# Optimization experiments

Measured on AMD Instinct MI355X. Metric: run time of the kernel, lower is better.

The kernel has to match this reference:

```python
import jax, jax.numpy as jnp
import numpy as np

ALPHAS = [2.0 ** k for k in range(-3, 2)]  # cfg.model.mmd.alphas = 2.0
EPS = 1e-12


def _center(x):
    return x - x.mean(axis=-1, keepdims=True)


def _l2norm(x):
    return x / jnp.sqrt(jnp.sum(x * x, axis=-1, keepdims=True) + EPS)


def _multi_gauss(d2):
    # sum_a exp(-a * d2), fused over the alpha list
    out = jnp.exp(-ALPHAS[0] * d2)
    for a in ALPHAS[1:]:
        out = out + jnp.exp(-a * d2)
    return out


def _sq_dists_self(x):
    # x: [..., n, c] -> squared euclidean pairwise [..., n, n]
    sq = jnp.sum(x * x, axis=-1)  # [..., n]
    gram = jnp.einsum('...ic,...jc->...ij', x, x)
    d2 = sq[..., :, None] + sq[..., None, :] - 2.0 * gram
    return jnp.maximum(d2, 0.0)


def setup_inputs() -> dict:
    key = jax.random.key(0)
    k1, k2 = jax.random.split(key)
    support_xf = jax.random.normal(k1, (16, 5, 130, 640), dtype=jnp.float32)
    query_xf = jax.random.normal(k2, (16, 75, 25, 640), dtype=jnp.float32)
    return {"support_xf": support_xf, "query_xf": query_xf}


def reference(support_xf, query_xf):
    # support_xf: [b, n_way, ns, c], query_xf: [b, q, nq, c]
    b, n_way, ns, c = support_xf.shape
    _, q, nq, _ = query_xf.shape

    # centering over feature dim, then l2 norm (cfg.model.mmd.l2norm = True)
    s = _l2norm(_center(support_xf))
    t = _l2norm(_center(query_xf))

    # self Gram kernels
    k_ss = _multi_gauss(_sq_dists_self(s))  # [b, n_way, ns, ns]
    k_qq = _multi_gauss(_sq_dists_self(t))  # [b, q, nq, nq]

    # cross kernel: broadcast instead of materializing expanded 5D copies
    sn = jnp.sum(s * s, axis=-1)  # [b, n_way, ns]
    tn = jnp.sum(t * t, axis=-1)  # [b, q, nq]
    gram_qs = jnp.einsum('bwsc,bqtc->bqwst', s, t)  # [b, q, n_way, ns, nq]
    d2_qs = jnp.maximum(
        sn[:, None, :, :, None] + tn[:, :, None, None, :] - 2.0 * gram_qs, 0.0)
    k_qs = _multi_gauss(d2_qs)

    # MMD terms: unbiased self terms drop the diagonal
    mmd_s = (jnp.sum(k_ss, axis=(-1, -2)) - jnp.trace(k_ss, axis1=-2, axis2=-1)) \
        / (ns * (ns - 1))  # [b, n_way]
    mmd_q = (jnp.sum(k_qq, axis=(-1, -2)) - jnp.trace(k_qq, axis1=-2, axis2=-1)) \
        / (nq * (nq - 1))  # [b, q]
    mmd_qs = jnp.sum(k_qs, axis=(-1, -2)) / (ns * nq)  # [b, q, n_way]

    mmd_dis = mmd_s[:, None, :] + mmd_q[:, :, None] - 2.0 * mmd_qs  # [b, q, n_way]
    return mmd_dis
```

## Files before the change

kernel.cpp:

```cpp
#include <hip/hip_runtime.h>
#include <math.h>


#define EXP_C (-0.25f * 1.44269504088896340736f)

typedef __attribute__((ext_vector_type(8))) short bf16x8_t;
typedef __attribute__((ext_vector_type(4))) float f32x4_t;
typedef unsigned short u16;

#define GLOAD_LDS16(g, l)                                 \
  __builtin_amdgcn_global_load_lds(                       \
      (const __attribute__((address_space(1))) void*)(g), \
      (__attribute__((address_space(3))) void*)(l), 16, 0, 0)

__device__ __forceinline__ u16 f2bf(float f) {
  unsigned int u = __float_as_uint(f);
  unsigned int r = (u + 0x7fffu + ((u >> 16) & 1u)) >> 16;
  return (u16)r;
}

__device__ __forceinline__ float mgauss(float g) {
  float h = fmaxf(1.f - g, 0.f);
  float e1 = exp2f(h * EXP_C);
  float e2 = e1 * e1, e4 = e2 * e2, e8 = e4 * e4, e16 = e8 * e8;
  return e1 + e2 + e4 + e8 + e16;
}

__device__ __forceinline__ float wred(float v) {
#pragma unroll
  for (int m = 1; m < 64; m <<= 1) v += __shfl_xor(v, m, 64);
  return v;
}

__global__ void prep_kernel(const float* __restrict__ S,
                            const float* __restrict__ Q,
                            u16* __restrict__ SHL, u16* __restrict__ QHL,
                            float* __restrict__ accz) {
  int bid = blockIdx.x, tid = threadIdx.x;
  if (bid < 29) {
    int z = bid * 256 + tid;
    if (z < 7280) accz[z] = 0.f;
  }
  int wid = (bid << 2) | (tid >> 6);
  int lane = tid & 63;
  const float* src;
  u16* dst;
  if (wid < 10400) {
    src = S + (size_t)wid * 640;
    dst = SHL + (size_t)wid * 640;
  } else {
    int w2 = wid - 10400;
    src = Q + (size_t)w2 * 640;
    dst = QHL + (size_t)w2 * 640;
  }
  const float4* s4 = (const float4*)src;
  float4 a = s4[lane];
  float4 b = s4[lane + 64];
  float4 c = make_float4(0.f, 0.f, 0.f, 0.f);
  if (lane < 32) c = s4[lane + 128];
  float s = a.x + a.y + a.z + a.w + b.x + b.y + b.z + b.w + c.x + c.y + c.z +
            c.w;
  float ss = a.x * a.x + a.y * a.y + a.z * a.z + a.w * a.w + b.x * b.x +
             b.y * b.y + b.z * b.z + b.w * b.w + c.x * c.x + c.y * c.y +
             c.z * c.z + c.w * c.w;
#pragma unroll
  for (int m = 1; m < 64; m <<= 1) {
    s += __shfl_xor(s, m, 64);
    ss += __shfl_xor(ss, m, 64);
  }
  float mean = s * (1.f / 640.f);
  float inv = 1.f / sqrtf(fmaxf(ss - s * s * (1.f / 640.f), 0.f) + 1e-12f);
  ushort4* d4 = (ushort4*)dst;
  d4[lane] = make_ushort4(f2bf((a.x - mean) * inv), f2bf((a.y - mean) * inv),
                          f2bf((a.z - mean) * inv), f2bf((a.w - mean) * inv));
  d4[lane + 64] =
      make_ushort4(f2bf((b.x - mean) * inv), f2bf((b.y - mean) * inv),
                   f2bf((b.z - mean) * inv), f2bf((b.w - mean) * inv));
  if (lane < 32)
    d4[lane + 128] =
        make_ushort4(f2bf((c.x - mean) * inv), f2bf((c.y - mean) * inv),
                     f2bf((c.z - mean) * inv), f2bf((c.w - mean) * inv));
}

__global__ __launch_bounds__(256, 2) void grams_kernel(
    const u16* __restrict__ SHL, const u16* __restrict__ QHL,
    float* __restrict__ accS, float* __restrict__ accQ,
    float* __restrict__ accQS) {
  __shared__ __align__(16) u16 sA[2][128 * 64];
  __shared__ __align__(16) u16 sB[2][128 * 64];
  const int bid = blockIdx.x;
  const int id = (bid & 7) * 242 + (bid >> 3);
  const int tid = threadIdx.x;
  const int w = tid >> 6, l = tid & 63;

  int mode, gb, i0, j0, nx, ny;
  const u16 *pX, *pY;
  if (id < 1440) {
    mode = 0;
    gb = id / 90;
    int r = id % 90;
    i0 = (r % 6) * 128;
    j0 = (r / 6) * 128;
    pX = SHL + (size_t)gb * 650 * 640;
    pY = QHL + (size_t)gb * 1875 * 640;
    nx = 650;
    ny = 1875;
  } else if (id < 1696) {
    mode = 1;
    int t = id - 1440;
    gb = t >> 4;
    int p = t & 15;
    int ti, tj;
    if (p < 4) {
      ti = p >> 1;
      tj = p & 1;
    } else {
      int q = (p - 4) / 3, r3 = (p - 4) % 3;
      ti = (r3 == 0) ? q + 1 : q + 2;
      tj = (r3 == 1) ? q + 1 : q + 2;
    }
    i0 = ti * 128;
    j0 = tj * 128;
    pX = pY = SHL + (size_t)gb * 650 * 640;
    nx = ny = 650;
  } else {
    mode = 2;
    gb = id - 1696;
    i0 = 0;
    j0 = 0;
    pX = pY = QHL + (size_t)gb * 125 * 640;
    nx = ny = 125;
  }

  const u16* gA[4];
  const u16* gB[4];
#pragma unroll
  for (int i = 0; i < 4; ++i) {
    int s = (w * 4 + i) * 64 + l;
    int r = s >> 3;
    int c16 = ((s & 7) ^ (r & 7)) * 8;
    int vi = i0 + r;
    vi = vi < nx ? vi : nx - 1;
    gA[i] = pX + (size_t)vi * 640 + c16;
    int vj = j0 + r;
    vj = vj < ny ? vj : ny - 1;
    gB[i] = pY + (size_t)vj * 640 + c16;
  }

  f32x4_t av[4][4];
#pragma unroll
  for (int i = 0; i < 4; ++i)
#pragma unroll
    for (int j = 0; j < 4; ++j)
#pragma unroll
      for (int r = 0; r < 4; ++r) av[i][j][r] = 0.f;

  const int wr = w >> 1, wc = w & 1;
  const int R0 = wr * 64, C0 = wc * 64;
  const int lr = l & 15, lk8 = (l >> 4) * 8;

#define STAGE(bb, c)                                          \
  {                                                           \
    int kb = (c) * 64;                                        \
    _Pragma("unroll") for (int i = 0; i < 4; ++i) {           \
      GLOAD_LDS16(gA[i] + kb, &sA[bb][(w * 4 + i) * 512]);    \
      GLOAD_LDS16(gB[i] + kb, &sB[bb][(w * 4 + i) * 512]);    \
    }                                                         \
  }

#define COMPUTE(bb)                                                           \
  {                                                                           \
    _Pragma("unroll") for (int ks = 0; ks < 2; ++ks) {                        \
      bf16x8_t af[4], bfv[4];                                                 \
      int kk = ks * 32 + lk8;                                                 \
      _Pragma("unroll") for (int t = 0; t < 4; ++t) {                         \
        int rr = R0 + t * 16 + lr;                                            \
        af[t] = *(const bf16x8_t*)&sA[bb][rr * 64 + (kk ^ ((rr & 7) << 3))];  \
        int cc = C0 + t * 16 + lr;                                            \
        bfv[t] = *(const bf16x8_t*)&sB[bb][cc * 64 + (kk ^ ((cc & 7) << 3))]; \
      }                                                                       \
      _Pragma("unroll") for (int i = 0; i < 4; ++i)                           \
          _Pragma("unroll") for (int j = 0; j < 4; ++j) av[i][j] =            \
          __builtin_amdgcn_mfma_f32_16x16x32_bf16(af[i], bfv[j], av[i][j], 0, \
                                                  0, 0);                      \
    }                                                                         \
  }

  STAGE(0, 0);
  __syncthreads();
  for (int c = 0; c < 10; ++c) {
    if (c < 9) STAGE((c + 1) & 1, c + 1);
    COMPUTE(c & 1);
    __syncthreads();
  }
#undef STAGE
#undef COMPUTE

  int gcv[4];
  bool cvv[4];
#pragma unroll
  for (int j = 0; j < 4; ++j) {
    gcv[j] = j0 + C0 + j * 16 + lr;
    cvv[j] = gcv[j] < ny;
  }

  if (mode == 0) {
    const int cbi = (i0 + R0) / 130;
    const int cbj = (j0 + C0) / 25;
    int cjr[4];
#pragma unroll
    for (int j = 0; j < 4; ++j) cjr[j] = gcv[j] / 25 - cbj;
    float ce[2][4] = {{0.f, 0.f, 0.f, 0.f}, {0.f, 0.f, 0.f, 0.f}};
#pragma unroll
    for (int i = 0; i < 4; ++i)
#pragma unroll
      for (int rr = 0; rr < 4; ++rr) {
        int gr = i0 + R0 + i * 16 + (l >> 4) * 4 + rr;
        bool rv = gr < 650;
        bool ra = (gr / 130) == cbi;
#pragma unroll
        for (int j = 0; j < 4; ++j) {
          float kv = mgauss(av[i][j][rr]);
          kv = (rv && cvv[j]) ? kv : 0.f;
          float k0 = ra ? kv : 0.f;
          ce[0][j] += k0;
          ce[1][j] += kv - k0;
        }
      }
#pragma unroll
    for (int a = 0; a < 2; ++a)
#pragma unroll
      for (int bq = 0; bq < 4; ++bq) {
        float t = 0.f;
#pragma unroll
        for (int j = 0; j < 4; ++j) t += (cjr[j] == bq) ? ce[a][j] : 0.f;
        t = wred(t);
        if (l == 0) {
          int ci = cbi + a, cj = cbj + bq;
          if (ci < 5 && cj < 75) atomicAdd(&accQS[gb * 375 + cj * 5 + ci], t);
        }
      }
  } else if (mode == 1) {
    const int cbi = (i0 + R0) / 130;
    int ccv[4];
#pragma unroll
    for (int j = 0; j < 4; ++j) ccv[j] = gcv[j] / 130;
    float ce[2][4] = {{0.f, 0.f, 0.f, 0.f}, {0.f, 0.f, 0.f, 0.f}};
#pragma unroll
    for (int i = 0; i < 4; ++i)
#pragma unroll
      for (int rr = 0; rr < 4; ++rr) {
        int gr = i0 + R0 + i * 16 + (l >> 4) * 4 + rr;
        bool rv = gr < 650;
        int rc = gr / 130;
        bool ra = rc == cbi;
#pragma unroll
        for (int j = 0; j < 4; ++j) {
          float kv = mgauss(av[i][j][rr]);
          bool val = rv && cvv[j] && (ccv[j] == rc) && (gr != gcv[j]);
          kv = val ? kv : 0.f;
          float k0 = ra ? kv : 0.f;
          ce[0][j] += k0;
          ce[1][j] += kv - k0;
        }
      }
#pragma unroll
    for (int a = 0; a < 2; ++a) {
      float t = wred(ce[a][0] + ce[a][1] + ce[a][2] + ce[a][3]);
      if (l == 0) {
        int ci = cbi + a;
        if (ci < 5) atomicAdd(&accS[gb * 5 + ci], t);
      }
    }
  } else {
    const int cbi = R0 / 25;
    int ccv[4];
#pragma unroll
    for (int j = 0; j < 4; ++j) ccv[j] = gcv[j] / 25;
    float ce[4][4] = {{0.f, 0.f, 0.f, 0.f},
                      {0.f, 0.f, 0.f, 0.f},
                      {0.f, 0.f, 0.f, 0.f},
                      {0.f, 0.f, 0.f, 0.f}};
#pragma unroll
    for (int i = 0; i < 4; ++i)
#pragma unroll
      for (int rr = 0; rr < 4; ++rr) {
        int gr = R0 + i * 16 + (l >> 4) * 4 + rr;
        bool rv = gr < 125;
        int rc = gr / 25;
        int ar = rc - cbi;
#pragma unroll
        for (int j = 0; j < 4; ++j) {
          float kv = mgauss(av[i][j][rr]);
          bool val = rv && cvv[j] && (ccv[j] == rc) && (gr != gcv[j]);
          kv = val ? kv : 0.f;
#pragma unroll
          for (int a = 0; a < 4; ++a) ce[a][j] += (ar == a) ? kv : 0.f;
        }
      }
#pragma unroll
    for (int a = 0; a < 4; ++a) {
      float t = wred(ce[a][0] + ce[a][1] + ce[a][2] + ce[a][3]);
      if (l == 0) {
        int ci = cbi + a;
        if (ci < 5) atomicAdd(&accQ[gb * 5 + ci], t);
      }
    }
  }
}

__global__ void finalize_kernel(const float* __restrict__ accS,
                                const float* __restrict__ accQ,
                                const float* __restrict__ accQS,
                                float* __restrict__ out) {
  int t = blockIdx.x * blockDim.x + threadIdx.x;
  if (t >= 6000) return;
  int w = t % 5;
  int bq = t / 5;
  int b = t / 375;
  out[t] = accS[b * 5 + w] * (1.f / (130.f * 129.f)) +
           accQ[bq] * (1.f / (25.f * 24.f)) - accQS[t] * (2.f / (130.f * 25.f));
}

extern "C" void kernel_launch(void* const* d_in, const int* in_sizes, int n_in,
                              void* d_out, int out_size, void* d_ws,
                              size_t ws_size, hipStream_t stream) {
  const float* S = (const float*)d_in[0];
  const float* Q = (const float*)d_in[1];
  float* ws = (float*)d_ws;
  float* accS = ws + 0;
  float* accQ = ws + 80;
  float* accQS = ws + 1280;
  u16* SHL = (u16*)(ws + 7280);
  u16* QHL = SHL + (size_t)10400 * 640;
  float* out = (float*)d_out;

  prep_kernel<<<10100, 256, 0, stream>>>(S, Q, SHL, QHL, ws);
  grams_kernel<<<1936, 256, 0, stream>>>(SHL, QHL, accS, accQ, accQS);
  finalize_kernel<<<24, 256, 0, stream>>>(accS, accQ, accQS, out);
}
```

Baseline: 216.0 us.

## Use 256x256 cross tiles with 512-thread blocks and fold finalize into last block

The cross-kernel Gram tiles grow from 128x128 to 256x256, computed by 8 waves per 512-thread block, which halves the LDS reloads of operands per output element. The self-kernel tiles keep 128x128 but are now split across 8 waves. The separate finalize launch is removed: a global atomic counter picks the last block, which computes the output, and the counter is zeroed together with the accumulators in the prep kernel. The larger tiles need more registers and LDS (64KB), which lowers occupancy, and there are fewer blocks (880) to balance across CUs.

```diff
diff --git a/kernel.cpp b/kernel.cpp
--- a/kernel.cpp
+++ b/kernel.cpp
@@ -39,7 +39,7 @@
   int bid = blockIdx.x, tid = threadIdx.x;
   if (bid < 29) {
     int z = bid * 256 + tid;
-    if (z < 7280) accz[z] = 0.f;
+    if (z < 7296) accz[z] = 0.f;
   }
   int wid = (bid << 2) | (tid >> 6);
   int lane = tid & 63;
@@ -82,137 +82,97 @@
                      f2bf((c.z - mean) * inv), f2bf((c.w - mean) * inv));
 }
 
-__global__ __launch_bounds__(256, 2) void grams_kernel(
+__global__ __launch_bounds__(512, 2) void mmd_kernel(
     const u16* __restrict__ SHL, const u16* __restrict__ QHL,
     float* __restrict__ accS, float* __restrict__ accQ,
-    float* __restrict__ accQS) {
-  __shared__ __align__(16) u16 sA[2][128 * 64];
-  __shared__ __align__(16) u16 sB[2][128 * 64];
+    float* __restrict__ accQS, int* __restrict__ ctr,
+    float* __restrict__ out) {
+  __shared__ __align__(16) u16 sA[2][256 * 64];
+  __shared__ __align__(16) u16 sB[2][256 * 64];
+  __shared__ int lastflag;
   const int bid = blockIdx.x;
-  const int id = (bid & 7) * 242 + (bid >> 3);
+  const int id = (bid & 7) * 110 + (bid >> 3);
   const int tid = threadIdx.x;
   const int w = tid >> 6, l = tid & 63;
-
-  int mode, gb, i0, j0, nx, ny;
-  const u16 *pX, *pY;
-  if (id < 1440) {
-    mode = 0;
-    gb = id / 90;
-    int r = id % 90;
-    i0 = (r % 6) * 128;
-    j0 = (r / 6) * 128;
-    pX = SHL + (size_t)gb * 650 * 640;
-    pY = QHL + (size_t)gb * 1875 * 640;
-    nx = 650;
-    ny = 1875;
-  } else if (id < 1696) {
-    mode = 1;
-    int t = id - 1440;
-    gb = t >> 4;
-    int p = t & 15;
-    int ti, tj;
-    if (p < 4) {
-      ti = p >> 1;
-      tj = p & 1;
-    } else {
-      int q = (p - 4) / 3, r3 = (p - 4) % 3;
-      ti = (r3 == 0) ? q + 1 : q + 2;
-      tj = (r3 == 1) ? q + 1 : q + 2;
-    }
-    i0 = ti * 128;
-    j0 = tj * 128;
-    pX = pY = SHL + (size_t)gb * 650 * 640;
-    nx = ny = 650;
-  } else {
-    mode = 2;
-    gb = id - 1696;
-    i0 = 0;
-    j0 = 0;
-    pX = pY = QHL + (size_t)gb * 125 * 640;
-    nx = ny = 125;
-  }
-
-  const u16* gA[4];
-  const u16* gB[4];
-#pragma unroll
-  for (int i = 0; i < 4; ++i) {
-    int s = (w * 4 + i) * 64 + l;
-    int r = s >> 3;
-    int c16 = ((s & 7) ^ (r & 7)) * 8;
-    int vi = i0 + r;
-    vi = vi < nx ? vi : nx - 1;
-    gA[i] = pX + (size_t)vi * 640 + c16;
-    int vj = j0 + r;
-    vj = vj < ny ? vj : ny - 1;
-    gB[i] = pY + (size_t)vj * 640 + c16;
-  }
-
-  f32x4_t av[4][4];
-#pragma unroll
-  for (int i = 0; i < 4; ++i)
-#pragma unroll
-    for (int j = 0; j < 4; ++j)
-#pragma unroll
-      for (int r = 0; r < 4; ++r) av[i][j][r] = 0.f;
-
-  const int wr = w >> 1, wc = w & 1;
-  const int R0 = wr * 64, C0 = wc * 64;
   const int lr = l & 15, lk8 = (l >> 4) * 8;
 
-#define STAGE(bb, c)                                          \
-  {                                                           \
-    int kb = (c) * 64;                                        \
-    _Pragma("unroll") for (int i = 0; i < 4; ++i) {           \
-      GLOAD_LDS16(gA[i] + kb, &sA[bb][(w * 4 + i) * 512]);    \
-      GLOAD_LDS16(gB[i] + kb, &sB[bb][(w * 4 + i) * 512]);    \
-    }                                                         \
-  }
-
-#define COMPUTE(bb)                                                           \
+  if (id < 384) {
+    const int gb = id / 24;
+    const int r = id % 24;
+    const int i0 = (r % 3) * 256, j0 = (r / 3) * 256;
+    const u16* pX = SHL + (size_t)gb * 650 * 640;
+    const u16* pY = QHL + (size_t)gb * 1875 * 640;
+    const u16 *gA[4], *gB[4];
+#pragma unroll
+    for (int i = 0; i < 4; ++i) {
+      int s = (w * 4 + i) * 64 + l;
+      int rw = s >> 3;
+      int c16 = ((s & 7) ^ (rw & 7)) * 8;
+      int vi = i0 + rw;
+      vi = vi < 650 ? vi : 649;
+      gA[i] = pX + (size_t)vi * 640 + c16;
+      int vj = j0 + rw;
+      vj = vj < 1875 ? vj : 1874;
+      gB[i] = pY + (size_t)vj * 640 + c16;
+    }
+    const int R0 = (w >> 2) * 128, C0 = (w & 3) * 64;
+    f32x4_t av[8][4];
+#pragma unroll
+    for (int i = 0; i < 8; ++i)
+#pragma unroll
+      for (int j = 0; j < 4; ++j)
+#pragma unroll
+        for (int q = 0; q < 4; ++q) av[i][j][q] = 0.f;
+
+#define STG0(bb, c)                                         \
+  {                                                         \
+    int kb = (c) * 64;                                      \
+    _Pragma("unroll") for (int i = 0; i < 4; ++i) {         \
+      GLOAD_LDS16(gA[i] + kb, &sA[bb][(w * 4 + i) * 512]);  \
+      GLOAD_LDS16(gB[i] + kb, &sB[bb][(w * 4 + i) * 512]);  \
+    }                                                       \
+  }
+#define CMP0(bb)                                                              \
   {                                                                           \
     _Pragma("unroll") for (int ks = 0; ks < 2; ++ks) {                        \
-      bf16x8_t af[4], bfv[4];                                                 \
+      bf16x8_t af[8], bfv[4];                                                 \
       int kk = ks * 32 + lk8;                                                 \
-      _Pragma("unroll") for (int t = 0; t < 4; ++t) {                         \
+      _Pragma("unroll") for (int t = 0; t < 8; ++t) {                         \
         int rr = R0 + t * 16 + lr;                                            \
         af[t] = *(const bf16x8_t*)&sA[bb][rr * 64 + (kk ^ ((rr & 7) << 3))];  \
+      }                                                                       \
+      _Pragma("unroll") for (int t = 0; t < 4; ++t) {                         \
         int cc = C0 + t * 16 + lr;                                            \
         bfv[t] = *(const bf16x8_t*)&sB[bb][cc * 64 + (kk ^ ((cc & 7) << 3))]; \
       }                                                                       \
-      _Pragma("unroll") for (int i = 0; i < 4; ++i)                           \
+      _Pragma("unroll") for (int i = 0; i < 8; ++i)                           \
           _Pragma("unroll") for (int j = 0; j < 4; ++j) av[i][j] =            \
           __builtin_amdgcn_mfma_f32_16x16x32_bf16(af[i], bfv[j], av[i][j], 0, \
                                                   0, 0);                      \
     }                                                                         \
   }
-
-  STAGE(0, 0);
-  __syncthreads();
-  for (int c = 0; c < 10; ++c) {
-    if (c < 9) STAGE((c + 1) & 1, c + 1);
-    COMPUTE(c & 1);
+    STG0(0, 0);
     __syncthreads();
-  }
-#undef STAGE
-#undef COMPUTE
-
-  int gcv[4];
-  bool cvv[4];
-#pragma unroll
-  for (int j = 0; j < 4; ++j) {
-    gcv[j] = j0 + C0 + j * 16 + lr;
-    cvv[j] = gcv[j] < ny;
-  }
-
-  if (mode == 0) {
+    for (int c = 0; c < 10; ++c) {
+      if (c < 9) STG0((c + 1) & 1, c + 1);
+      CMP0(c & 1);
+      __syncthreads();
+    }
+#undef STG0
+#undef CMP0
     const int cbi = (i0 + R0) / 130;
     const int cbj = (j0 + C0) / 25;
-    int cjr[4];
-#pragma unroll
-    for (int j = 0; j < 4; ++j) cjr[j] = gcv[j] / 25 - cbj;
+    int gcv[4], cjr[4];
+    bool cvv[4];
+#pragma unroll
+    for (int j = 0; j < 4; ++j) {
+      gcv[j] = j0 + C0 + j * 16 + lr;
+      cvv[j] = gcv[j] < 1875;
+      cjr[j] = gcv[j] / 25 - cbj;
+    }
     float ce[2][4] = {{0.f, 0.f, 0.f, 0.f}, {0.f, 0.f, 0.f, 0.f}};
 #pragma unroll
-    for (int i = 0; i < 4; ++i)
+    for (int i = 0; i < 8; ++i)
 #pragma unroll
       for (int rr = 0; rr < 4; ++rr) {
         int gr = i0 + R0 + i * 16 + (l >> 4) * 4 + rr;
@@ -240,86 +200,184 @@
           if (ci < 5 && cj < 75) atomicAdd(&accQS[gb * 375 + cj * 5 + ci], t);
         }
       }
-  } else if (mode == 1) {
-    const int cbi = (i0 + R0) / 130;
-    int ccv[4];
-#pragma unroll
-    for (int j = 0; j < 4; ++j) ccv[j] = gcv[j] / 130;
-    float ce[2][4] = {{0.f, 0.f, 0.f, 0.f}, {0.f, 0.f, 0.f, 0.f}};
+  } else {
+    int mode, gb, i0, j0, nx;
+    const u16* pX;
+    if (id < 640) {
+      mode = 1;
+      int t = id - 384;
+      gb = t >> 4;
+      int p = t & 15;
+      int ti, tj;
+      if (p < 4) {
+        ti = p >> 1;
+        tj = p & 1;
+      } else {
+        int q = (p - 4) / 3, r3 = (p - 4) % 3;
+        ti = (r3 == 0) ? q + 1 : q + 2;
+        tj = (r3 == 1) ? q + 1 : q + 2;
+      }
+      i0 = ti * 128;
+      j0 = tj * 128;
+      pX = SHL + (size_t)gb * 650 * 640;
+      nx = 650;
+    } else {
+      mode = 2;
+      gb = id - 640;
+      i0 = 0;
+      j0 = 0;
+      pX = QHL + (size_t)gb * 125 * 640;
+      nx = 125;
+    }
+    const u16 *gA[2], *gB[2];
+#pragma unroll
+    for (int i = 0; i < 2; ++i) {
+      int s = i * 512 + tid;
+      int rw = s >> 3;
+      int c16 = ((s & 7) ^ (rw & 7)) * 8;
+      int vi = i0 + rw;
+      vi = vi < nx ? vi : nx - 1;
+      gA[i] = pX + (size_t)vi * 640 + c16;
+      int vj = j0 + rw;
+      vj = vj < nx ? vj : nx - 1;
+      gB[i] = pX + (size_t)vj * 640 + c16;
+    }
+    const int R0 = (w >> 2) * 64, C0 = (w & 3) * 32;
+    f32x4_t av[4][2];
 #pragma unroll
     for (int i = 0; i < 4; ++i)
 #pragma unroll
-      for (int rr = 0; rr < 4; ++rr) {
-        int gr = i0 + R0 + i * 16 + (l >> 4) * 4 + rr;
-        bool rv = gr < 650;
-        int rc = gr / 130;
-        bool ra = rc == cbi;
-#pragma unroll
-        for (int j = 0; j < 4; ++j) {
-          float kv = mgauss(av[i][j][rr]);
-          bool val = rv && cvv[j] && (ccv[j] == rc) && (gr != gcv[j]);
-          kv = val ? kv : 0.f;
-          float k0 = ra ? kv : 0.f;
-          ce[0][j] += k0;
-          ce[1][j] += kv - k0;
-        }
-      }
-#pragma unroll
-    for (int a = 0; a < 2; ++a) {
-      float t = wred(ce[a][0] + ce[a][1] + ce[a][2] + ce[a][3]);
-      if (l == 0) {
-        int ci = cbi + a;
-        if (ci < 5) atomicAdd(&accS[gb * 5 + ci], t);
-      }
-    }
-  } else {
-    const int cbi = R0 / 25;
-    int ccv[4];
-#pragma unroll
-    for (int j = 0; j < 4; ++j) ccv[j] = gcv[j] / 25;
-    float ce[4][4] = {{0.f, 0.f, 0.f, 0.f},
-                      {0.f, 0.f, 0.f, 0.f},
-                      {0.f, 0.f, 0.f, 0.f},
-                      {0.f, 0.f, 0.f, 0.f}};
-#pragma unroll
-    for (int i = 0; i < 4; ++i)
-#pragma unroll
-      for (int rr = 0; rr < 4; ++rr) {
-        int gr = R0 + i * 16 + (l >> 4) * 4 + rr;
-        bool rv = gr < 125;
-        int rc = gr / 25;
-        int ar = rc - cbi;
-#pragma unroll
-        for (int j = 0; j < 4; ++j) {
-          float kv = mgauss(av[i][j][rr]);
-          bool val = rv && cvv[j] && (ccv[j] == rc) && (gr != gcv[j]);
-          kv = val ? kv : 0.f;
-#pragma unroll
-          for (int a = 0; a < 4; ++a) ce[a][j] += (ar == a) ? kv : 0.f;
-        }
-      }
-#pragma unroll
-    for (int a = 0; a < 4; ++a) {
-      float t = wred(ce[a][0] + ce[a][1] + ce[a][2] + ce[a][3]);
-      if (l == 0) {
-        int ci = cbi + a;
-        if (ci < 5) atomicAdd(&accQ[gb * 5 + ci], t);
-      }
-    }
-  }
-}
-
-__global__ void finalize_kernel(const float* __restrict__ accS,
-                                const float* __restrict__ accQ,
-                                const float* __restrict__ accQS,
-                                float* __restrict__ out) {
-  int t = blockIdx.x * blockDim.x + threadIdx.x;
-  if (t >= 6000) return;
-  int w = t % 5;
-  int bq = t / 5;
-  int b = t / 375;
-  out[t] = accS[b * 5 + w] * (1.f / (130.f * 129.f)) +
-           accQ[bq] * (1.f / (25.f * 24.f)) - accQS[t] * (2.f / (130.f * 25.f));
+      for (int j = 0; j < 2; ++j)
+#pragma unroll
+        for (int q = 0; q < 4; ++q) av[i][j][q] = 0.f;
+
+#define STG1(bb, c)                                        \
+  {                                                        \
+    int kb = (c) * 64;                                     \
+    _Pragma("unroll") for (int i = 0; i < 2; ++i) {        \
+      GLOAD_LDS16(gA[i] + kb, &sA[bb][(i * 8 + w) * 512]); \
+      GLOAD_LDS16(gB[i] + kb, &sB[bb][(i * 8 + w) * 512]); \
+    }                                                      \
+  }
+#define CMP1(bb)                                                              \
+  {                                                                           \
+    _Pragma("unroll") for (int ks = 0; ks < 2; ++ks) {                        \
+      bf16x8_t af[4], bfv[2];                                                 \
+      int kk = ks * 32 + lk8;                                                 \
+      _Pragma("unroll") for (int t = 0; t < 4; ++t) {                         \
+        int rr = R0 + t * 16 + lr;                                            \
+        af[t] = *(const bf16x8_t*)&sA[bb][rr * 64 + (kk ^ ((rr & 7) << 3))];  \
+      }                                                                       \
+      _Pragma("unroll") for (int t = 0; t < 2; ++t) {                         \
+        int cc = C0 + t * 16 + lr;                                            \
+        bfv[t] = *(const bf16x8_t*)&sB[bb][cc * 64 + (kk ^ ((cc & 7) << 3))]; \
+      }                                                                       \
+      _Pragma("unroll") for (int i = 0; i < 4; ++i)                           \
+          _Pragma("unroll") for (int j = 0; j < 2; ++j) av[i][j] =            \
+          __builtin_amdgcn_mfma_f32_16x16x32_bf16(af[i], bfv[j], av[i][j], 0, \
+                                                  0, 0);                      \
+    }                                                                         \
+  }
+    STG1(0, 0);
+    __syncthreads();
+    for (int c = 0; c < 10; ++c) {
+      if (c < 9) STG1((c + 1) & 1, c + 1);
+      CMP1(c & 1);
+      __syncthreads();
+    }
+#undef STG1
+#undef CMP1
+    int gcv[2], ccv[2];
+    bool cvv[2];
+#pragma unroll
+    for (int j = 0; j < 2; ++j) {
+      gcv[j] = j0 + C0 + j * 16 + lr;
+      cvv[j] = gcv[j] < nx;
+    }
+    if (mode == 1) {
+      const int cbi = (i0 + R0) / 130;
+#pragma unroll
+      for (int j = 0; j < 2; ++j) ccv[j] = gcv[j] / 130;
+      float ce[2] = {0.f, 0.f};
+#pragma unroll
+      for (int i = 0; i < 4; ++i)
+#pragma unroll
+        for (int rr = 0; rr < 4; ++rr) {
+          int gr = i0 + R0 + i * 16 + (l >> 4) * 4 + rr;
+          bool rv = gr < 650;
+          int rc = gr / 130;
+          bool ra = rc == cbi;
+#pragma unroll
+          for (int j = 0; j < 2; ++j) {
+            float kv = mgauss(av[i][j][rr]);
+            bool val = rv && cvv[j] && (ccv[j] == rc) && (gr != gcv[j]);
+            kv = val ? kv : 0.f;
+            float k0 = ra ? kv : 0.f;
+            ce[0] += k0;
+            ce[1] += kv - k0;
+          }
+        }
+#pragma unroll
+      for (int a = 0; a < 2; ++a) {
+        float t = wred(ce[a]);
+        if (l == 0) {
+          int ci = cbi + a;
+          if (ci < 5) atomicAdd(&accS[gb * 5 + ci], t);
+        }
+      }
+    } else {
+      const int cbi = R0 / 25;
+#pragma unroll
+      for (int j = 0; j < 2; ++j) ccv[j] = gcv[j] / 25;
+      float ce[4] = {0.f, 0.f, 0.f, 0.f};
+#pragma unroll
+      for (int i = 0; i < 4; ++i)
+#pragma unroll
+        for (int rr = 0; rr < 4; ++rr) {
+          int gr = R0 + i * 16 + (l >> 4) * 4 + rr;
+          bool rv = gr < 125;
+          int rc = gr / 25;
+          int ar = rc - cbi;
+#pragma unroll
+          for (int j = 0; j < 2; ++j) {
+            float kv = mgauss(av[i][j][rr]);
+            bool val = rv && cvv[j] && (ccv[j] == rc) && (gr != gcv[j]);
+            kv = val ? kv : 0.f;
+#pragma unroll
+            for (int a = 0; a < 4; ++a) ce[a] += (ar == a) ? kv : 0.f;
+          }
+        }
+#pragma unroll
+      for (int a = 0; a < 4; ++a) {
+        float t = wred(ce[a]);
+        if (l == 0) {
+          int ci = cbi + a;
+          if (ci < 5) atomicAdd(&accQ[gb * 5 + ci], t);
+        }
+      }
+    }
+  }
+
+  __threadfence();
+  if (tid == 0) {
+    int old = __hip_atomic_fetch_add(ctr, 1, __ATOMIC_ACQ_REL,
+                                     __HIP_MEMORY_SCOPE_AGENT);
+    lastflag = (old == 879) ? 1 : 0;
+  }
+  __syncthreads();
+  if (lastflag) {
+    for (int k = tid; k < 6000; k += 512) {
+      int w5 = k % 5, bq = k / 5, b = k / 375;
+      float aS = __hip_atomic_load(&accS[b * 5 + w5], __ATOMIC_RELAXED,
+                                   __HIP_MEMORY_SCOPE_AGENT);
+      float aQ = __hip_atomic_load(&accQ[bq], __ATOMIC_RELAXED,
+                                   __HIP_MEMORY_SCOPE_AGENT);
+      float aQS = __hip_atomic_load(&accQS[k], __ATOMIC_RELAXED,
+                                    __HIP_MEMORY_SCOPE_AGENT);
+      out[k] = aS * (1.f / (130.f * 129.f)) + aQ * (1.f / (25.f * 24.f)) -
+               aQS * (2.f / (130.f * 25.f));
+    }
+  }
 }
 
 extern "C" void kernel_launch(void* const* d_in, const int* in_sizes, int n_in,
@@ -331,11 +389,11 @@
   float* accS = ws + 0;
   float* accQ = ws + 80;
   float* accQS = ws + 1280;
-  u16* SHL = (u16*)(ws + 7280);
+  int* ctr = (int*)(ws + 7280);
+  u16* SHL = (u16*)(ws + 7296);
   u16* QHL = SHL + (size_t)10400 * 640;
   float* out = (float*)d_out;
 
   prep_kernel<<<10100, 256, 0, stream>>>(S, Q, SHL, QHL, ws);
-  grams_kernel<<<1936, 256, 0, stream>>>(SHL, QHL, accS, accQ, accQS);
-  finalize_kernel<<<24, 256, 0, stream>>>(accS, accQ, accQS, out);
-}
+  mmd_kernel<<<880, 512, 0, stream>>>(SHL, QHL, accS, accQ, accQS, ctr, out);
+}
```

Result: slower. 430.8 us (+99.5%).
